# Optimization experiments

Hardware: AMD Instinct MI355X
Metric: run time of the kernel (lower is better)

## Reference

```python
import jax, jax.numpy as jnp
import numpy as np

NUM_BITS = 8
VMIN, VMAX = 0.0, 1.0
THRESH = 4.0
K_SYN = 32


def gray_code_encode(x):
    # (batch, features) -> (batch, features*NUM_BITS) binary float bits
    norm = (jnp.clip(x, VMIN, VMAX) - VMIN) / (VMAX - VMIN)
    levels = jnp.round(norm * (2 ** NUM_BITS - 1)).astype(jnp.int32)
    gray = levels ^ (levels >> 1)
    bit_pos = jnp.arange(NUM_BITS, dtype=jnp.int32)
    bits = ((gray[..., None] >> bit_pos) & 1).astype(jnp.float32)
    return bits.reshape(x.shape[0], -1)


def _make_sparse_weight(key, n_neurons, prev_size):
    # k random synapses per neuron with +/-1 weights (rest zero), as in
    # _initialise_layer_weights (standard, non-dynamic path)
    kc, ks = jax.random.split(key)
    cols = jax.random.randint(kc, (n_neurons, K_SYN), 0, prev_size)
    signs = jax.random.randint(ks, (n_neurons, K_SYN), 0, 2).astype(jnp.float32) * 2 - 1
    rows = jnp.broadcast_to(jnp.arange(n_neurons)[:, None], (n_neurons, K_SYN))
    return jnp.zeros((n_neurons, prev_size), jnp.float32).at[rows, cols].set(signs)


def setup_inputs() -> dict:
    key = jax.random.key(0)
    kx, k0, k1, k2, ko = jax.random.split(key, 5)
    batch, feat = 512, 256
    hidden, classes, n_hidden_layers = 4096, 1000, 3
    enc = feat * NUM_BITS  # 2048
    x = jax.random.uniform(kx, (batch, feat), dtype=jnp.float32)
    W0 = _make_sparse_weight(k0, hidden, enc)
    W1 = _make_sparse_weight(k1, hidden, hidden)
    W2 = _make_sparse_weight(k2, hidden, hidden)
    out_w = jax.random.normal(ko, (n_hidden_layers, hidden, classes), dtype=jnp.float32) * 0.01
    return {"x": x, "W0": W0, "W1": W1, "W2": W2, "out_w": out_w}


def reference(x, W0, W1, W2, out_w):
    prev = gray_code_encode(x)  # (b, enc)
    out = jnp.zeros((x.shape[0], out_w.shape[-1]), jnp.float32)
    for i, W in enumerate((W0, W1, W2)):
        z = prev @ W.T                                  # (b, hidden)
        prev = (z >= THRESH).astype(jnp.float32)        # binary activation
        out = out + prev @ out_w[i]                     # accumulate per-layer
    return out
```

## Files before the change

### kernel.cpp

```cpp
#include <hip/hip_runtime.h>
#include <stdint.h>

typedef unsigned long long u64;
typedef __attribute__((ext_vector_type(8))) short bf16x8;
typedef __attribute__((ext_vector_type(4))) float f32x4;
typedef __attribute__((ext_vector_type(4))) unsigned u32x4;

#define BATCH 512
#define FEAT 256
#define ENC 2048
#define HID 4096
#define CLS 1000
#define KTOT 12288
#define KSPLIT 768

#define OFF_ENC2   0
#define OFF_ACT2   131072
#define OFF_TABLE  917504
#define OFF_SGN    1703936
#define OFF_WT     2097152

static __device__ inline unsigned short f2bf(float f) {
    unsigned u = __float_as_uint(f);
    return (unsigned short)((u + 0x7FFFu + ((u >> 16) & 1u)) >> 16);
}

static __device__ inline void gld16(const void* g, void* s) {
    __builtin_amdgcn_global_load_lds((const __attribute__((address_space(1))) void*)g,
                                     (__attribute__((address_space(3))) void*)s, 16, 0, 0);
}

__global__ void __launch_bounds__(256)
k_prep(const float* __restrict__ x, u64* __restrict__ enc2,
       const float* __restrict__ W0, const float* __restrict__ W1,
       const float* __restrict__ W2,
       uint16_t* __restrict__ table, unsigned* __restrict__ bits,
       const float* __restrict__ out_w, short* __restrict__ wt,
       float* __restrict__ out) {
    __shared__ short tile[64 * 68];
    int bid = blockIdx.x;
    int t = threadIdx.x;
    int lane = t & 63;
    int wv = t >> 6;

    if (bid < 512) {
        int oidx = bid * 256 + t;
        if (oidx < (BATCH * CLS) / 4) {
            f32x4 z = {0.f, 0.f, 0.f, 0.f};
            *(f32x4*)&out[(size_t)oidx * 4] = z;
        }
        int wid = bid * 4 + wv;
        int f = wid >> 3, bg = wid & 7;
        float v = x[(size_t)(bg * 64 + lane) * FEAT + f];
        v = fminf(fmaxf(v, 0.0f), 1.0f);
        int lev = (int)rintf(v * 255.0f);
        unsigned gray = (unsigned)(lev ^ (lev >> 1));
        u64 w = 0;
        #pragma unroll
        for (int bit = 0; bit < 8; ++bit) {
            u64 m = __ballot((gray >> bit) & 1u);
            if (lane == bit) w = m;
        }
        if (lane < 8) enc2[(size_t)bg * ENC + f * 8 + lane] = w;
        return;
    }
    if (bid < 3584) {
        int row = (bid - 512) * 4 + wv;
        const float* Wr; int npass;
        if (row < HID)          { Wr = W0 + (size_t)row * ENC;             npass = 1; }
        else if (row < 2 * HID) { Wr = W1 + (size_t)(row - HID) * HID;     npass = 2; }
        else                    { Wr = W2 + (size_t)(row - 2 * HID) * HID; npass = 2; }
        uint16_t* te = table + (size_t)row * 32;
        unsigned cnt = 0, mynegs = 0;
        u64 ltmask = (1ull << lane) - 1ull;
        for (int p = 0; p < npass; ++p) {
            const u32x4* p4 = (const u32x4*)Wr + p * 512 + lane;
            u32x4 v[8];
            #pragma unroll
            for (int j = 0; j < 8; ++j) v[j] = __builtin_nontemporal_load(p4 + j * 64);
            #pragma unroll
            for (int j = 0; j < 8; ++j) {
                int col0 = (p * 8 + j) * 256 + lane * 4;
                unsigned aa[4] = {v[j].x, v[j].y, v[j].z, v[j].w};
                #pragma unroll
                for (int c = 0; c < 4; ++c) {
                    unsigned a = aa[c];
                    u64 m = __ballot(a != 0u);
                    if (a) {
                        int slot = (int)cnt + (int)__popcll(m & ltmask);
                        te[slot] = (uint16_t)(col0 + c);
                        if (a >> 31) mynegs |= 1u << slot;
                    }
                    cnt += (unsigned)__popcll(m);
                }
            }
        }
        #pragma unroll
        for (int off = 32; off; off >>= 1) mynegs |= __shfl_xor(mynegs, off);
        if (lane >= (int)cnt && lane < 32) te[lane] = 0;
        if (lane == 0) {
            uint2 pr;
            pr.x = mynegs;
            pr.y = (cnt >= 32) ? 0xFFFFFFFFu : ((1u << cnt) - 1u);
            *(uint2*)(bits + (size_t)row * 2) = pr;
        }
        return;
    }
    {
        int b2 = bid - 3584;
        int kt = b2 % 192, ct = b2 / 192;
        int k0 = kt * 64, c0 = ct * 64;
        {
            int rrow = t >> 4, c4 = t & 15;
            int c = c0 + c4 * 4;
            #pragma unroll
            for (int rd = 0; rd < 4; ++rd) {
                int kl = rd * 16 + rrow;
                f32x4 vv;
                if (c < CLS)
                    vv = __builtin_nontemporal_load(
                        (const f32x4*)&out_w[(size_t)(k0 + kl) * CLS + c]);
                else { vv.x = 0.0f; vv.y = 0.0f; vv.z = 0.0f; vv.w = 0.0f; }
                short* d = &tile[kl * 68 + c4 * 4];
                d[0] = (short)f2bf(vv.x); d[1] = (short)f2bf(vv.y);
                d[2] = (short)f2bf(vv.z); d[3] = (short)f2bf(vv.w);
            }
        }
        __syncthreads();
        {
            int chunk = t & 7, cl2 = t >> 3;
            #pragma unroll
            for (int rd = 0; rd < 2; ++rd) {
                int c_local = rd * 32 + cl2;
                int c = c0 + c_local;
                unsigned s8[8];
                #pragma unroll
                for (int j = 0; j < 8; ++j)
                    s8[j] = (unsigned)(unsigned short)tile[(chunk * 8 + j) * 68 + c_local];
                uint4 pk;
                pk.x = s8[0] | (s8[1] << 16);
                pk.y = s8[2] | (s8[3] << 16);
                pk.z = s8[4] | (s8[5] << 16);
                pk.w = s8[6] | (s8[7] << 16);
                *(uint4*)&wt[(size_t)c * KTOT + k0 + ((chunk ^ (c & 7)) * 8)] = pk;
            }
        }
    }
}

static __device__ __forceinline__ u64 unit_csa(
    const u64* __restrict__ prow,
    const uint16_t* __restrict__ table_l, const unsigned* __restrict__ bits_l, int n) {
    const uint4* tq = (const uint4*)(table_l + (size_t)n * 32);
    uint4 cwa[4] = {tq[0], tq[1], tq[2], tq[3]};
    uint2 bv = *(const uint2*)(bits_l + (size_t)n * 2);
    unsigned negb = bv.x, valb = bv.y;

    u64 P[4][4];
    #pragma unroll
    for (int k = 0; k < 4; ++k) {
        unsigned w0 = cwa[k].x, w1 = cwa[k].y, w2 = cwa[k].z, w3 = cwa[k].w;
        unsigned cc[8] = { w0 & 0xFFFFu, w0 >> 16, w1 & 0xFFFFu, w1 >> 16,
                           w2 & 0xFFFFu, w2 >> 16, w3 & 0xFFFFu, w3 >> 16 };
        u64 u[8];
        #pragma unroll
        for (int e = 0; e < 8; ++e) {
            int j = (k << 3) + e;
            u64 w = prow[cc[e]];
            u64 negm = 0ull - (u64)((negb >> j) & 1u);
            u64 vm   = 0ull - (u64)((valb >> j) & 1u);
            u[e] = (w ^ negm) & vm;
        }
        u64 s0, c0, s1, c1, s2, c2, b0, c3, t2, d0, b1, d1;
        { u64 t = u[0] ^ u[1]; s0 = t ^ u[2]; c0 = (u[0] & u[1]) | (u[2] & t); }
        { u64 t = u[3] ^ u[4]; s1 = t ^ u[5]; c1 = (u[3] & u[4]) | (u[5] & t); }
        s2 = u[6] ^ u[7]; c2 = u[6] & u[7];
        { u64 t = s0 ^ s1; b0 = t ^ s2; c3 = (s0 & s1) | (s2 & t); }
        { u64 t = c0 ^ c1; t2 = t ^ c2; d0 = (c0 & c1) | (c2 & t); }
        b1 = t2 ^ c3; d1 = t2 & c3;
        P[k][0] = b0; P[k][1] = b1; P[k][2] = d0 ^ d1; P[k][3] = d0 & d1;
    }
    u64 A[5], B[5], U[6];
    { u64 c;
      { u64 t = P[0][0] ^ P[1][0]; A[0] = t; c = P[0][0] & P[1][0]; }
      #pragma unroll
      for (int i = 1; i < 4; ++i) {
          u64 t = P[0][i] ^ P[1][i]; A[i] = t ^ c; c = (P[0][i] & P[1][i]) | (c & t); }
      A[4] = c; }
    { u64 c;
      { u64 t = P[2][0] ^ P[3][0]; B[0] = t; c = P[2][0] & P[3][0]; }
      #pragma unroll
      for (int i = 1; i < 4; ++i) {
          u64 t = P[2][i] ^ P[3][i]; B[i] = t ^ c; c = (P[2][i] & P[3][i]) | (c & t); }
      B[4] = c; }
    { u64 c;
      { u64 t = A[0] ^ B[0]; U[0] = t; c = A[0] & B[0]; }
      #pragma unroll
      for (int i = 1; i < 5; ++i) {
          u64 t = A[i] ^ B[i]; U[i] = t ^ c; c = (A[i] & B[i]) | (c & t); }
      U[5] = c; }
    int K = 60 - __popc(negb & valb);
    u64 c = 0;
    #pragma unroll
    for (int i = 0; i < 6; ++i) {
        u64 ki = 0ull - (u64)((K >> i) & 1);
        u64 t = U[i] ^ ki;
        c = (U[i] & ki) | (c & t);
    }
    return c;
}

__global__ void __launch_bounds__(64)
k_layer(const u64* __restrict__ prev2, int Kwords,
        const uint16_t* __restrict__ table_l, const unsigned* __restrict__ bits_l,
        u64* __restrict__ actout) {
    int unit = blockIdx.x;
    int lane = threadIdx.x;
    int g = unit >> 3, bg = unit & 7;
    int n = (g << 6) + lane;
    u64 c = unit_csa(prev2 + (size_t)bg * Kwords, table_l, bits_l, n);
    actout[(size_t)bg * HID + n] = c;
}

__global__ void __launch_bounds__(256)
k_gemm_atomic(const u64* __restrict__ act2, const short* __restrict__ wt,
              float* __restrict__ out) {
    __shared__ __attribute__((aligned(16))) short As[64 * 64];
    __shared__ __attribute__((aligned(16))) short Bs[128 * 64];
    int bid = blockIdx.x;
    int nt = bid & 7, ks = (bid >> 3) & 15, mt = bid >> 7;
    int tid = threadIdx.x, lane = tid & 63;
    int wv = tid >> 6;
    int quad = lane >> 4, cl = lane & 15;
    f32x4 acc[4][2] = {};
    const char* Bb = (const char*)(wt + (size_t)nt * 128 * KTOT + ks * KSPLIT);
    int r = tid >> 3, sub = tid & 7;
    for (int kk = 0; kk < KSPLIT; kk += 64) {
        #pragma unroll
        for (int rd = 0; rd < 4; ++rd) {
            size_t go = (size_t)(r + rd * 32) * (KTOT * 2) + kk * 2 + sub * 16;
            gld16(Bb + go, &Bs[(tid + rd * 256) * 8]);
        }
        {
            int kabs = ks * KSPLIT + kk;
            int l = kabs >> 12, nk = kabs & 4095;
            #pragma unroll
            for (int i = 0; i < 2; ++i) {
                int item = i * 256 + tid;
                int rr = item >> 3, gg = item & 7;
                const u64* w8 = act2 + ((size_t)(l * 8 + mt)) * HID + nk + gg * 8;
                unsigned sh[8];
                #pragma unroll
                for (int j = 0; j < 8; ++j)
                    sh[j] = (unsigned)((w8[j] >> rr) & 1ull) * 0x3F80u;
                uint4 pk;
                pk.x = sh[0] | (sh[1] << 16);
                pk.y = sh[2] | (sh[3] << 16);
                pk.z = sh[4] | (sh[5] << 16);
                pk.w = sh[6] | (sh[7] << 16);
                *(uint4*)&As[rr * 64 + ((gg ^ (rr & 7)) * 8)] = pk;
            }
        }
        __syncthreads();
        #pragma unroll
        for (int s = 0; s < 2; ++s) {
            int xr = ((s * 4 + quad) ^ (cl & 7)) * 8;
            bf16x8 af[4], bfr[2];
            #pragma unroll
            for (int mf = 0; mf < 4; ++mf)
                af[mf] = *(const bf16x8*)&As[(mf * 16 + cl) * 64 + xr];
            #pragma unroll
            for (int nf = 0; nf < 2; ++nf)
                bfr[nf] = *(const bf16x8*)&Bs[(wv * 32 + nf * 16 + cl) * 64 + xr];
            #pragma unroll
            for (int mf = 0; mf < 4; ++mf)
                #pragma unroll
                for (int nf = 0; nf < 2; ++nf)
                    acc[mf][nf] = __builtin_amdgcn_mfma_f32_16x16x32_bf16(
                        af[mf], bfr[nf], acc[mf][nf], 0, 0, 0);
        }
        __syncthreads();
    }
    #pragma unroll
    for (int mf = 0; mf < 4; ++mf)
        #pragma unroll
        for (int nf = 0; nf < 2; ++nf) {
            int cp = nt * 128 + wv * 32 + nf * 16 + cl;
            if (cp < CLS) {
                #pragma unroll
                for (int rr = 0; rr < 4; ++rr) {
                    int mg = mt * 64 + mf * 16 + quad * 4 + rr;
                    atomicAdd(&out[(size_t)mg * CLS + cp], acc[mf][nf][rr]);
                }
            }
        }
}

extern "C" void kernel_launch(void* const* d_in, const int* in_sizes, int n_in,
                              void* d_out, int out_size, void* d_ws, size_t ws_size,
                              hipStream_t stream) {
    const float* x     = (const float*)d_in[0];
    const float* W0    = (const float*)d_in[1];
    const float* W1    = (const float*)d_in[2];
    const float* W2    = (const float*)d_in[3];
    const float* out_w = (const float*)d_in[4];
    float* out = (float*)d_out;
    char* ws = (char*)d_ws;

    u64*       enc2   = (u64*)(ws + OFF_ENC2);
    u64*       act2   = (u64*)(ws + OFF_ACT2);
    uint16_t*  table  = (uint16_t*)(ws + OFF_TABLE);
    unsigned*  bits   = (unsigned*)(ws + OFF_SGN);
    short*     wt     = (short*)(ws + OFF_WT);

    hipLaunchKernelGGL(k_prep, dim3(6656), dim3(256), 0, stream,
                       x, enc2, W0, W1, W2, table, bits, out_w, wt, out);
    hipLaunchKernelGGL(k_layer, dim3(512), dim3(64), 0, stream,
                       enc2, ENC, table, bits, act2);
    hipLaunchKernelGGL(k_layer, dim3(512), dim3(64), 0, stream,
                       act2, HID, table + (size_t)HID * 32, bits + (size_t)HID * 2,
                       act2 + 8 * HID);
    hipLaunchKernelGGL(k_layer, dim3(512), dim3(64), 0, stream,
                       act2 + 8 * HID, HID, table + (size_t)2 * HID * 32,
                       bits + (size_t)2 * HID * 2, act2 + 16 * HID);
    hipLaunchKernelGGL(k_gemm_atomic, dim3(1024), dim3(256), 0, stream,
                       act2, wt, out);
}
```

Measured before the change: 270.4 us.

## Fuse three layer kernels with per-batch-group atomic barriers; double-buffer GEMM tiles

Replaces the three per-layer launches with one kernel whose blocks sync per batch group through global atomic counters. Counters are zeroed in the prep kernel, so launch gaps between layers go away. The output GEMM now double-buffers its A and B shared-memory tiles, prefetching the next K slice while MFMAs run on the current one. The spin-wait assumes all 512 small blocks are co-resident, which is a deadlock risk, and the doubled LDS use may lower occupancy.

```diff
diff --git a/kernel.cpp b/kernel.cpp
--- a/kernel.cpp
+++ b/kernel.cpp
@@ -18,6 +18,7 @@
 #define OFF_ACT2   131072
 #define OFF_TABLE  917504
 #define OFF_SGN    1703936
+#define OFF_CNT    1802240
 #define OFF_WT     2097152
 
 static __device__ inline unsigned short f2bf(float f) {
@@ -36,7 +37,7 @@
        const float* __restrict__ W2,
        uint16_t* __restrict__ table, unsigned* __restrict__ bits,
        const float* __restrict__ out_w, short* __restrict__ wt,
-       float* __restrict__ out) {
+       float* __restrict__ out, int* __restrict__ sync) {
     __shared__ short tile[64 * 68];
     int bid = blockIdx.x;
     int t = threadIdx.x;
@@ -44,6 +45,7 @@
     int wv = t >> 6;
 
     if (bid < 512) {
+        if (bid == 0) { sync[t] = 0; sync[t + 256] = 0; }
         int oidx = bid * 256 + t;
         if (oidx < (BATCH * CLS) / 4) {
             f32x4 z = {0.f, 0.f, 0.f, 0.f};
@@ -211,22 +213,43 @@
 }
 
 __global__ void __launch_bounds__(64)
-k_layer(const u64* __restrict__ prev2, int Kwords,
-        const uint16_t* __restrict__ table_l, const unsigned* __restrict__ bits_l,
-        u64* __restrict__ actout) {
+k_layers3(const u64* __restrict__ enc2, const uint16_t* __restrict__ table,
+          const unsigned* __restrict__ bits, u64* __restrict__ act2,
+          int* __restrict__ sync) {
     int unit = blockIdx.x;
     int lane = threadIdx.x;
     int g = unit >> 3, bg = unit & 7;
     int n = (g << 6) + lane;
-    u64 c = unit_csa(prev2 + (size_t)bg * Kwords, table_l, bits_l, n);
-    actout[(size_t)bg * HID + n] = c;
+
+    u64 c = unit_csa(enc2 + (size_t)bg * ENC, table, bits, n);
+    act2[(size_t)bg * HID + n] = c;
+    if (lane == 0)
+        __hip_atomic_fetch_add(&sync[bg * 32], 1, __ATOMIC_RELEASE,
+                               __HIP_MEMORY_SCOPE_AGENT);
+    while (__hip_atomic_load(&sync[bg * 32], __ATOMIC_ACQUIRE,
+                             __HIP_MEMORY_SCOPE_AGENT) < 64)
+        __builtin_amdgcn_s_sleep(8);
+
+    c = unit_csa(act2 + (size_t)bg * HID, table + (size_t)HID * 32,
+                 bits + (size_t)HID * 2, n);
+    act2[(size_t)(8 + bg) * HID + n] = c;
+    if (lane == 0)
+        __hip_atomic_fetch_add(&sync[(8 + bg) * 32], 1, __ATOMIC_RELEASE,
+                               __HIP_MEMORY_SCOPE_AGENT);
+    while (__hip_atomic_load(&sync[(8 + bg) * 32], __ATOMIC_ACQUIRE,
+                             __HIP_MEMORY_SCOPE_AGENT) < 64)
+        __builtin_amdgcn_s_sleep(8);
+
+    c = unit_csa(act2 + (size_t)(8 + bg) * HID, table + (size_t)2 * HID * 32,
+                 bits + (size_t)2 * HID * 2, n);
+    act2[(size_t)(16 + bg) * HID + n] = c;
 }
 
 __global__ void __launch_bounds__(256)
 k_gemm_atomic(const u64* __restrict__ act2, const short* __restrict__ wt,
               float* __restrict__ out) {
-    __shared__ __attribute__((aligned(16))) short As[64 * 64];
-    __shared__ __attribute__((aligned(16))) short Bs[128 * 64];
+    __shared__ __attribute__((aligned(16))) short As[2][64 * 64];
+    __shared__ __attribute__((aligned(16))) short Bs[2][128 * 64];
     int bid = blockIdx.x;
     int nt = bid & 7, ks = (bid >> 3) & 15, mt = bid >> 7;
     int tid = threadIdx.x, lane = tid & 63;
@@ -234,44 +257,62 @@
     int quad = lane >> 4, cl = lane & 15;
     f32x4 acc[4][2] = {};
     const char* Bb = (const char*)(wt + (size_t)nt * 128 * KTOT + ks * KSPLIT);
-    int r = tid >> 3, sub = tid & 7;
-    for (int kk = 0; kk < KSPLIT; kk += 64) {
+    int r = tid >> 3, sub = tid & 7, gg = tid & 7;
+    u64 aw[8];
+
+    auto STAGE_B = [&](int kk, int buf) {
         #pragma unroll
         for (int rd = 0; rd < 4; ++rd) {
             size_t go = (size_t)(r + rd * 32) * (KTOT * 2) + kk * 2 + sub * 16;
-            gld16(Bb + go, &Bs[(tid + rd * 256) * 8]);
-        }
-        {
-            int kabs = ks * KSPLIT + kk;
-            int l = kabs >> 12, nk = kabs & 4095;
-            #pragma unroll
-            for (int i = 0; i < 2; ++i) {
-                int item = i * 256 + tid;
-                int rr = item >> 3, gg = item & 7;
-                const u64* w8 = act2 + ((size_t)(l * 8 + mt)) * HID + nk + gg * 8;
-                unsigned sh[8];
-                #pragma unroll
-                for (int j = 0; j < 8; ++j)
-                    sh[j] = (unsigned)((w8[j] >> rr) & 1ull) * 0x3F80u;
-                uint4 pk;
-                pk.x = sh[0] | (sh[1] << 16);
-                pk.y = sh[2] | (sh[3] << 16);
-                pk.z = sh[4] | (sh[5] << 16);
-                pk.w = sh[6] | (sh[7] << 16);
-                *(uint4*)&As[rr * 64 + ((gg ^ (rr & 7)) * 8)] = pk;
-            }
-        }
-        __syncthreads();
+            gld16(Bb + go, &Bs[buf][(tid + rd * 256) * 8]);
+        }
+    };
+    auto LOAD_A = [&](int kk) {
+        int kabs = ks * KSPLIT + kk;
+        int l = kabs >> 12, nk = kabs & 4095;
+        const u64* base = act2 + ((size_t)(l * 8 + mt)) * HID + nk + gg * 8;
+        #pragma unroll
+        for (int j = 0; j < 8; ++j) aw[j] = base[j];
+    };
+    auto PACK_A = [&](int buf) {
+        #pragma unroll
+        for (int i = 0; i < 2; ++i) {
+            int rr = i * 32 + (tid >> 3);
+            unsigned sh[8];
+            #pragma unroll
+            for (int j = 0; j < 8; ++j)
+                sh[j] = (unsigned)((aw[j] >> rr) & 1ull) * 0x3F80u;
+            uint4 pk;
+            pk.x = sh[0] | (sh[1] << 16);
+            pk.y = sh[2] | (sh[3] << 16);
+            pk.z = sh[4] | (sh[5] << 16);
+            pk.w = sh[6] | (sh[7] << 16);
+            *(uint4*)&As[buf][rr * 64 + ((gg ^ (rr & 7)) * 8)] = pk;
+        }
+    };
+
+    STAGE_B(0, 0);
+    LOAD_A(0);
+    PACK_A(0);
+    __syncthreads();
+
+    int cur = 0;
+    for (int kk = 0; kk < KSPLIT; kk += 64) {
+        int nxt = kk + 64;
+        if (nxt < KSPLIT) {
+            STAGE_B(nxt, cur ^ 1);
+            LOAD_A(nxt);
+        }
         #pragma unroll
         for (int s = 0; s < 2; ++s) {
             int xr = ((s * 4 + quad) ^ (cl & 7)) * 8;
             bf16x8 af[4], bfr[2];
             #pragma unroll
             for (int mf = 0; mf < 4; ++mf)
-                af[mf] = *(const bf16x8*)&As[(mf * 16 + cl) * 64 + xr];
+                af[mf] = *(const bf16x8*)&As[cur][(mf * 16 + cl) * 64 + xr];
             #pragma unroll
             for (int nf = 0; nf < 2; ++nf)
-                bfr[nf] = *(const bf16x8*)&Bs[(wv * 32 + nf * 16 + cl) * 64 + xr];
+                bfr[nf] = *(const bf16x8*)&Bs[cur][(wv * 32 + nf * 16 + cl) * 64 + xr];
             #pragma unroll
             for (int mf = 0; mf < 4; ++mf)
                 #pragma unroll
@@ -279,8 +320,11 @@
                     acc[mf][nf] = __builtin_amdgcn_mfma_f32_16x16x32_bf16(
                         af[mf], bfr[nf], acc[mf][nf], 0, 0, 0);
         }
+        if (nxt < KSPLIT) PACK_A(cur ^ 1);
         __syncthreads();
-    }
+        cur ^= 1;
+    }
+
     #pragma unroll
     for (int mf = 0; mf < 4; ++mf)
         #pragma unroll
@@ -311,18 +355,13 @@
     u64*       act2   = (u64*)(ws + OFF_ACT2);
     uint16_t*  table  = (uint16_t*)(ws + OFF_TABLE);
     unsigned*  bits   = (unsigned*)(ws + OFF_SGN);
+    int*       sync   = (int*)(ws + OFF_CNT);
     short*     wt     = (short*)(ws + OFF_WT);
 
     hipLaunchKernelGGL(k_prep, dim3(6656), dim3(256), 0, stream,
-                       x, enc2, W0, W1, W2, table, bits, out_w, wt, out);
-    hipLaunchKernelGGL(k_layer, dim3(512), dim3(64), 0, stream,
-                       enc2, ENC, table, bits, act2);
-    hipLaunchKernelGGL(k_layer, dim3(512), dim3(64), 0, stream,
-                       act2, HID, table + (size_t)HID * 32, bits + (size_t)HID * 2,
-                       act2 + 8 * HID);
-    hipLaunchKernelGGL(k_layer, dim3(512), dim3(64), 0, stream,
-                       act2 + 8 * HID, HID, table + (size_t)2 * HID * 32,
-                       bits + (size_t)2 * HID * 2, act2 + 16 * HID);
+                       x, enc2, W0, W1, W2, table, bits, out_w, wt, out, sync);
+    hipLaunchKernelGGL(k_layers3, dim3(512), dim3(64), 0, stream,
+                       enc2, table, bits, act2, sync);
     hipLaunchKernelGGL(k_gemm_atomic, dim3(1024), dim3(256), 0, stream,
                        act2, wt, out);
 }
```

After: 302.1 us. +11.7%, slower.

## Load GEMM operands straight into registers, dropping LDS staging and swizzle

Applied to the files above, without the earlier changes.

The output GEMM no longer stages A and B tiles through shared memory. Each lane now loads its B fragment directly from the transposed weight buffer and builds its bf16 A fragment in registers from the packed activation bit-words. The prep kernel stops XOR-swizzling the weight layout to match. This removes the LDS writes, bank-conflict handling and both __syncthreads per k-step, but each wave now re-reads global memory without sharing data across the block, so it relies on cache hits and may lose load coalescing.

```diff
diff --git a/kernel.cpp b/kernel.cpp
--- a/kernel.cpp
+++ b/kernel.cpp
@@ -23,11 +23,6 @@
 static __device__ inline unsigned short f2bf(float f) {
     unsigned u = __float_as_uint(f);
     return (unsigned short)((u + 0x7FFFu + ((u >> 16) & 1u)) >> 16);
-}
-
-static __device__ inline void gld16(const void* g, void* s) {
-    __builtin_amdgcn_global_load_lds((const __attribute__((address_space(1))) void*)g,
-                                     (__attribute__((address_space(3))) void*)s, 16, 0, 0);
 }
 
 __global__ void __launch_bounds__(256)
@@ -142,7 +137,7 @@
                 pk.y = s8[2] | (s8[3] << 16);
                 pk.z = s8[4] | (s8[5] << 16);
                 pk.w = s8[6] | (s8[7] << 16);
-                *(uint4*)&wt[(size_t)c * KTOT + k0 + ((chunk ^ (c & 7)) * 8)] = pk;
+                *(uint4*)&wt[(size_t)c * KTOT + k0 + chunk * 8] = pk;
             }
         }
     }
@@ -223,64 +218,63 @@
 }
 
 __global__ void __launch_bounds__(256)
-k_gemm_atomic(const u64* __restrict__ act2, const short* __restrict__ wt,
+k_gemm_direct(const u64* __restrict__ act2, const short* __restrict__ wt,
               float* __restrict__ out) {
-    __shared__ __attribute__((aligned(16))) short As[64 * 64];
-    __shared__ __attribute__((aligned(16))) short Bs[128 * 64];
     int bid = blockIdx.x;
     int nt = bid & 7, ks = (bid >> 3) & 15, mt = bid >> 7;
     int tid = threadIdx.x, lane = tid & 63;
     int wv = tid >> 6;
     int quad = lane >> 4, cl = lane & 15;
     f32x4 acc[4][2] = {};
-    const char* Bb = (const char*)(wt + (size_t)nt * 128 * KTOT + ks * KSPLIT);
-    int r = tid >> 3, sub = tid & 7;
-    for (int kk = 0; kk < KSPLIT; kk += 64) {
-        #pragma unroll
-        for (int rd = 0; rd < 4; ++rd) {
-            size_t go = (size_t)(r + rd * 32) * (KTOT * 2) + kk * 2 + sub * 16;
-            gld16(Bb + go, &Bs[(tid + rd * 256) * 8]);
-        }
-        {
-            int kabs = ks * KSPLIT + kk;
-            int l = kabs >> 12, nk = kabs & 4095;
-            #pragma unroll
-            for (int i = 0; i < 2; ++i) {
-                int item = i * 256 + tid;
-                int rr = item >> 3, gg = item & 7;
-                const u64* w8 = act2 + ((size_t)(l * 8 + mt)) * HID + nk + gg * 8;
-                unsigned sh[8];
-                #pragma unroll
-                for (int j = 0; j < 8; ++j)
-                    sh[j] = (unsigned)((w8[j] >> rr) & 1ull) * 0x3F80u;
-                uint4 pk;
-                pk.x = sh[0] | (sh[1] << 16);
-                pk.y = sh[2] | (sh[3] << 16);
-                pk.z = sh[4] | (sh[5] << 16);
-                pk.w = sh[6] | (sh[7] << 16);
-                *(uint4*)&As[rr * 64 + ((gg ^ (rr & 7)) * 8)] = pk;
-            }
-        }
-        __syncthreads();
-        #pragma unroll
-        for (int s = 0; s < 2; ++s) {
-            int xr = ((s * 4 + quad) ^ (cl & 7)) * 8;
-            bf16x8 af[4], bfr[2];
-            #pragma unroll
-            for (int mf = 0; mf < 4; ++mf)
-                af[mf] = *(const bf16x8*)&As[(mf * 16 + cl) * 64 + xr];
-            #pragma unroll
-            for (int nf = 0; nf < 2; ++nf)
-                bfr[nf] = *(const bf16x8*)&Bs[(wv * 32 + nf * 16 + cl) * 64 + xr];
-            #pragma unroll
-            for (int mf = 0; mf < 4; ++mf)
-                #pragma unroll
-                for (int nf = 0; nf < 2; ++nf)
-                    acc[mf][nf] = __builtin_amdgcn_mfma_f32_16x16x32_bf16(
-                        af[mf], bfr[nf], acc[mf][nf], 0, 0, 0);
-        }
-        __syncthreads();
-    }
+    const short* Bc0 = wt + (size_t)(nt * 128 + wv * 32 + cl) * KTOT;
+    const short* Bc1 = Bc0 + (size_t)16 * KTOT;
+    const u64*   Arow = act2 + (size_t)mt * HID;
+    int kbase = ks * KSPLIT;
+
+    #pragma unroll 2
+    for (int t32 = 0; t32 < KSPLIT / 32; ++t32) {
+        int kabs = kbase + t32 * 32;
+        int l = kabs >> 12, nk = kabs & 4095;
+        const u64* aw = Arow + (size_t)l * (8 * HID) + nk + quad * 8;
+        u64 w[8];
+        #pragma unroll
+        for (int j = 0; j < 8; ++j) w[j] = aw[j];
+        bf16x8 bfr0 = *(const bf16x8*)&Bc0[kabs + quad * 8];
+        bf16x8 bfr1 = *(const bf16x8*)&Bc1[kabs + quad * 8];
+        unsigned tl[8], th[8];
+        #pragma unroll
+        for (int j = 0; j < 8; ++j) {
+            u64 t = w[j] >> cl;
+            tl[j] = (unsigned)t;
+            th[j] = (unsigned)(t >> 32);
+        }
+        bf16x8 af[4];
+        #pragma unroll
+        for (int mf = 0; mf < 4; ++mf) {
+            unsigned sh = (mf & 1) * 16;
+            uint4 pk;
+            if (mf < 2) {
+                pk.x = (((tl[0] >> sh) & 1u) | (((tl[1] >> sh) & 1u) << 16)) * 0x3F80u;
+                pk.y = (((tl[2] >> sh) & 1u) | (((tl[3] >> sh) & 1u) << 16)) * 0x3F80u;
+                pk.z = (((tl[4] >> sh) & 1u) | (((tl[5] >> sh) & 1u) << 16)) * 0x3F80u;
+                pk.w = (((tl[6] >> sh) & 1u) | (((tl[7] >> sh) & 1u) << 16)) * 0x3F80u;
+            } else {
+                pk.x = (((th[0] >> sh) & 1u) | (((th[1] >> sh) & 1u) << 16)) * 0x3F80u;
+                pk.y = (((th[2] >> sh) & 1u) | (((th[3] >> sh) & 1u) << 16)) * 0x3F80u;
+                pk.z = (((th[4] >> sh) & 1u) | (((th[5] >> sh) & 1u) << 16)) * 0x3F80u;
+                pk.w = (((th[6] >> sh) & 1u) | (((th[7] >> sh) & 1u) << 16)) * 0x3F80u;
+            }
+            af[mf] = *(bf16x8*)&pk;
+        }
+        #pragma unroll
+        for (int mf = 0; mf < 4; ++mf) {
+            acc[mf][0] = __builtin_amdgcn_mfma_f32_16x16x32_bf16(af[mf], bfr0,
+                                                                acc[mf][0], 0, 0, 0);
+            acc[mf][1] = __builtin_amdgcn_mfma_f32_16x16x32_bf16(af[mf], bfr1,
+                                                                acc[mf][1], 0, 0, 0);
+        }
+    }
+
     #pragma unroll
     for (int mf = 0; mf < 4; ++mf)
         #pragma unroll
@@ -323,6 +317,6 @@
     hipLaunchKernelGGL(k_layer, dim3(512), dim3(64), 0, stream,
                        act2 + 8 * HID, HID, table + (size_t)2 * HID * 32,
                        bits + (size_t)2 * HID * 2, act2 + 16 * HID);
-    hipLaunchKernelGGL(k_gemm_atomic, dim3(1024), dim3(256), 0, stream,
+    hipLaunchKernelGGL(k_gemm_direct, dim3(1024), dim3(256), 0, stream,
                        act2, wt, out);
 }
```

New measurement: 279.7 us. +3.5%, slower.
